# Optimization experiments

Measured on AMD Instinct MI355X. Metric: run time of the kernel, lower is better.

The kernel has to match this reference:

```python
import jax, jax.numpy as jnp
import numpy as np

H = 16            # num heads (sharded)
NOPE = 128        # qk_nope_head_dim
ROPE = 64         # qk_rope_head_dim
VD = 128          # v_head_dim
KV_RANK = 512
HEAD = NOPE + ROPE  # 192
SCALE = HEAD ** (-0.5)  # mscale == 1 (no yarn scaling)
EPS = 1e-6


def rmsnorm(x, w):
    var = jnp.mean(x * x, axis=-1, keepdims=True)
    return x * jax.lax.rsqrt(var + EPS) * w


def apply_rope(pe, cos, sin):
    # pe: [T, h, ROPE]; torch code de-interleaves pairs then applies
    # non-interleaved (rotate-half) rope: out = [e*cos - o*sin, o*cos + e*sin]
    e = pe[..., 0::2]
    o = pe[..., 1::2]
    c = cos[:, None, :]
    s = sin[:, None, :]
    return jnp.concatenate([e * c - o * s, o * c + e * s], axis=-1)


def setup_inputs() -> dict:
    key = jax.random.key(0)
    ks = jax.random.split(key, 10)
    T, D = 4096, 2048
    w = 0.02
    return {
        "hidden_states": jax.random.normal(ks[0], (T, D), jnp.float32),
        "cos": jax.random.uniform(ks[1], (T, ROPE // 2), jnp.float32),
        "sin": jax.random.uniform(ks[2], (T, ROPE // 2), jnp.float32),
        "w_q_a": jax.random.normal(ks[3], (D, 1536), jnp.float32) * w,
        "q_a_ln_w": jnp.ones((1536,), jnp.float32),
        "w_q_b": jax.random.normal(ks[4], (1536, H * HEAD), jnp.float32) * w,
        "w_kv_a": jax.random.normal(ks[5], (D, KV_RANK + ROPE), jnp.float32) * w,
        "kv_a_ln_w": jnp.ones((KV_RANK,), jnp.float32),
        "w_kv_b": jax.random.normal(ks[6], (KV_RANK, H * (NOPE + VD)), jnp.float32) * w,
        "w_o": jax.random.normal(ks[7], (H * VD, D), jnp.float32) * w,
        "batch_size": 2,
    }


def reference(hidden_states, cos, sin, w_q_a, q_a_ln_w, w_q_b, w_kv_a,
              kv_a_ln_w, w_kv_b, w_o, batch_size):
    T, D = hidden_states.shape
    B = int(batch_size)
    S = T // B

    # Q: low-rank down proj -> RMSNorm -> up proj
    q = rmsnorm(hidden_states @ w_q_a, q_a_ln_w) @ w_q_b
    q = q.reshape(T, H, HEAD)
    q_nope = q[..., :NOPE]
    q_pe = apply_rope(q[..., NOPE:], cos, sin)

    # KV: joint down proj with shared rope part (MQA-style)
    ckv = hidden_states @ w_kv_a                        # [T, 512+64]
    compressed_kv = ckv[:, :KV_RANK]
    k_pe = apply_rope(ckv[:, KV_RANK:][:, None, :], cos, sin)  # [T, 1, 64]
    kv = (rmsnorm(compressed_kv, kv_a_ln_w) @ w_kv_b).reshape(T, H, NOPE + VD)
    k_nope = kv[..., :NOPE]
    v = kv[..., NOPE:]                                   # [T, H, 128]

    # Assemble full query/key heads (value pad to 192 + final slice is a no-op
    # mathematically since padded dims are zero; we keep value dim = 128).
    query = jnp.concatenate([q_nope, q_pe], axis=-1)     # [T, H, 192]
    key = jnp.concatenate([k_nope, jnp.broadcast_to(k_pe, (T, H, ROPE))], axis=-1)

    # Causal (prefill) attention per sequence
    qb = query.reshape(B, S, H, HEAD)
    kb = key.reshape(B, S, H, HEAD)
    vb = v.reshape(B, S, H, VD)
    scores = jnp.einsum("bqhd,bkhd->bhqk", qb, kb) * SCALE
    causal = jnp.tril(jnp.ones((S, S), bool))
    scores = jnp.where(causal, scores, jnp.finfo(scores.dtype).min)
    probs = jax.nn.softmax(scores, axis=-1)
    attn = jnp.einsum("bhqk,bkhd->bqhd", probs, vb)      # [B, S, H, 128]

    return attn.reshape(T, H * VD) @ w_o
```

## Files before the change

### kernel.cpp

```cpp
#include <hip/hip_runtime.h>
#include <cstdint>
#include <cstddef>

#define TT 4096
#define DD 2048
#define NH 16
#define HEADD 192
#define NOPE 128
#define VDIM 128
#define SEQ 2048

typedef __bf16 bf16x8 __attribute__((ext_vector_type(8)));
typedef float f32x4 __attribute__((ext_vector_type(4)));
typedef unsigned int u32;

__device__ __forceinline__ float bf2f(unsigned short u) {
    union { unsigned int i; float f; } v; v.i = ((unsigned int)u) << 16; return v.f;
}
__device__ __forceinline__ unsigned short f2bf(float f) {
    union { float f; unsigned int i; } v; v.f = f;
    unsigned int r = v.i + 0x7FFFu + ((v.i >> 16) & 1u);
    return (unsigned short)(r >> 16);
}
__device__ __forceinline__ u32 pack2bf(float a, float b) {
    return (u32)f2bf(a) | ((u32)f2bf(b) << 16);
}
__device__ __forceinline__ void gload16(const unsigned short* g, unsigned short* l) {
    __builtin_amdgcn_global_load_lds((const __attribute__((address_space(1))) u32*)g,
                                     (__attribute__((address_space(3))) u32*)l, 16, 0, 0);
}

#define GMFMA __builtin_amdgcn_mfma_f32_16x16x32_bf16

__global__ __launch_bounds__(256) void cvt_bf16_k(const float* __restrict__ x,
                                                  unsigned short* __restrict__ y, int n) {
    int i = (blockIdx.x * 256 + threadIdx.x) * 4;
    if (i < n) {
        float4 v = *(const float4*)(x + i);
        uint2 o;
        o.x = pack2bf(v.x, v.y);
        o.y = pack2bf(v.z, v.w);
        *(uint2*)(y + i) = o;
    }
}

__global__ __launch_bounds__(256) void transpose_cvt_k(const float* __restrict__ W,
                                                       unsigned short* __restrict__ Wt,
                                                       int K, int N) {
    __shared__ float tile[32][33];
    int n0 = blockIdx.x * 32, k0 = blockIdx.y * 32;
    int t = threadIdx.x, lr = t >> 5, lc = t & 31;
#pragma unroll
    for (int p = 0; p < 4; p++) {
        int k = k0 + lr + p * 8, n = n0 + lc;
        tile[lr + p * 8][lc] = (k < K && n < N) ? W[(size_t)k * N + n] : 0.f;
    }
    __syncthreads();
#pragma unroll
    for (int p = 0; p < 4; p++) {
        int n = n0 + lr + p * 8, k = k0 + lc;
        if (n < N && k < K) Wt[(size_t)n * K + k] = f2bf(tile[lc][lr + p * 8]);
    }
}

template <int BN, typename OT>
__global__ __launch_bounds__(512) void gemm256_k(const unsigned short* __restrict__ A,
                                                 const unsigned short* __restrict__ Bt,
                                                 OT* __restrict__ C,
                                                 int M, int N, int K) {
    constexpr int NREP = BN / 64;
    constexpr int NB = BN / 64;
    constexpr int TILE_E = 8192 + BN * 64;
    __shared__ __align__(16) unsigned short lds[2 * TILE_E];
    const int t = threadIdx.x;
    const int w = t >> 6, lane = t & 63;
    const int wr = w >> 2, wc = w & 3;
    const int l15 = lane & 15, quad = lane >> 4;
    const int bm = blockIdx.y * 128, bn = blockIdx.x * BN;
    const int srow = w * 8 + (lane >> 3);
    const int scol = 8 * ((lane & 7) ^ (lane >> 3));
    const unsigned short* Ag = A + (size_t)(bm + srow) * K + scol;
    const unsigned short* Bg = Bt + (size_t)(bn + srow) * K + scol;
    const int rc0 = (quad * 8) ^ ((l15 & 7) * 8);
    const int rc1 = (32 + quad * 8) ^ ((l15 & 7) * 8);
    f32x4 acc[4][NREP];
    f32x4 zero = {0.f, 0.f, 0.f, 0.f};
#pragma unroll
    for (int i = 0; i < 4; i++)
#pragma unroll
        for (int n = 0; n < NREP; n++) acc[i][n] = zero;
    const int NT = K >> 6;
#pragma unroll
    for (int c = 0; c < 2; c++)
        gload16(Ag + (size_t)c * 64 * K, &lds[c * 4096 + w * 512]);
#pragma unroll
    for (int c = 0; c < NB; c++)
        gload16(Bg + (size_t)c * 64 * K, &lds[8192 + c * 4096 + w * 512]);

    for (int kt = 0; kt < NT; kt++) {
        const int cb = (kt & 1) * TILE_E;
        const int nb = TILE_E - cb;
        const bool more = (kt + 1) < NT;
        asm volatile("s_waitcnt vmcnt(0)" ::: "memory");
        __builtin_amdgcn_s_barrier();
        asm volatile("" ::: "memory");
        const unsigned short* Agk = Ag + (size_t)(kt + 1) * 64;
        const unsigned short* Bgk = Bg + (size_t)(kt + 1) * 64;
        if (more) {
            gload16(Agk, &lds[nb + w * 512]);
            gload16(Agk + (size_t)64 * K, &lds[nb + 4096 + w * 512]);
#pragma unroll
            for (int c = 0; c < NB / 2; c++)
                gload16(Bgk + (size_t)c * 64 * K, &lds[nb + 8192 + c * 4096 + w * 512]);
        }
        bf16x8 a0[2][2], b[NREP][2];
#pragma unroll
        for (int j = 0; j < 2; j++) {
            int rl = wr * 64 + j * 16 + l15;
            a0[j][0] = *(const bf16x8*)&lds[cb + rl * 64 + rc0];
            a0[j][1] = *(const bf16x8*)&lds[cb + rl * 64 + rc1];
        }
#pragma unroll
        for (int n = 0; n < NREP; n++) {
            int rl = wc * (BN / 4) + n * 16 + l15;
            b[n][0] = *(const bf16x8*)&lds[cb + 8192 + rl * 64 + rc0];
            b[n][1] = *(const bf16x8*)&lds[cb + 8192 + rl * 64 + rc1];
        }
        __builtin_amdgcn_s_setprio(1);
#pragma unroll
        for (int j = 0; j < 2; j++)
#pragma unroll
            for (int n = 0; n < NREP; n++) {
                acc[j][n] = GMFMA(a0[j][0], b[n][0], acc[j][n], 0, 0, 0);
                acc[j][n] = GMFMA(a0[j][1], b[n][1], acc[j][n], 0, 0, 0);
            }
        __builtin_amdgcn_s_setprio(0);
        __builtin_amdgcn_s_barrier();
        if (more) {
#pragma unroll
            for (int c = NB / 2; c < NB; c++)
                gload16(Bgk + (size_t)c * 64 * K, &lds[nb + 8192 + c * 4096 + w * 512]);
        }
        bf16x8 a1[2][2];
#pragma unroll
        for (int j = 0; j < 2; j++) {
            int rl = wr * 64 + 32 + j * 16 + l15;
            a1[j][0] = *(const bf16x8*)&lds[cb + rl * 64 + rc0];
            a1[j][1] = *(const bf16x8*)&lds[cb + rl * 64 + rc1];
        }
        __builtin_amdgcn_s_setprio(1);
#pragma unroll
        for (int j = 0; j < 2; j++)
#pragma unroll
            for (int n = 0; n < NREP; n++) {
                acc[2 + j][n] = GMFMA(a1[j][0], b[n][0], acc[2 + j][n], 0, 0, 0);
                acc[2 + j][n] = GMFMA(a1[j][1], b[n][1], acc[2 + j][n], 0, 0, 0);
            }
        __builtin_amdgcn_s_setprio(0);
    }
#pragma unroll
    for (int mi = 0; mi < 4; mi++) {
        int row = bm + wr * 64 + mi * 16 + quad * 4;
#pragma unroll
        for (int n = 0; n < NREP; n++) {
            int col = bn + wc * (BN / 4) + n * 16 + l15;
            OT* cp = C + (size_t)row * N + col;
#pragma unroll
            for (int r = 0; r < 4; r++) {
                float v = acc[mi][n][r];
                if constexpr (sizeof(OT) == 2) cp[(size_t)r * N] = f2bf(v);
                else                            cp[(size_t)r * N] = v;
            }
        }
    }
}

__global__ __launch_bounds__(512) void gemm192_rope_k(const unsigned short* __restrict__ A,
                                                      const unsigned short* __restrict__ Bt,
                                                      const float* __restrict__ cosb,
                                                      const float* __restrict__ sinb,
                                                      unsigned short* __restrict__ Qb) {
    constexpr int K = 1536, N = 3072;
    constexpr int NREP = 3, NB = 3;
    constexpr int TILE_E = 8192 + 192 * 64;
    __shared__ __align__(16) unsigned short lds[2 * TILE_E];
    const int t = threadIdx.x;
    const int w = t >> 6, lane = t & 63;
    const int wr = w >> 2, wc = w & 3;
    const int l15 = lane & 15, quad = lane >> 4;
    const int bm = blockIdx.y * 128, bn = blockIdx.x * 192;
    const int srow = w * 8 + (lane >> 3);
    const int scol = 8 * ((lane & 7) ^ (lane >> 3));
    const unsigned short* Ag = A + (size_t)(bm + srow) * K + scol;
    const unsigned short* Bg = Bt + (size_t)(bn + srow) * K + scol;
    const int rc0 = (quad * 8) ^ ((l15 & 7) * 8);
    const int rc1 = (32 + quad * 8) ^ ((l15 & 7) * 8);
    f32x4 acc[4][NREP];
    f32x4 zero = {0.f, 0.f, 0.f, 0.f};
#pragma unroll
    for (int i = 0; i < 4; i++)
#pragma unroll
        for (int n = 0; n < NREP; n++) acc[i][n] = zero;
    const int NT = K >> 6;
#pragma unroll
    for (int c = 0; c < 2; c++)
        gload16(Ag + (size_t)c * 64 * K, &lds[c * 4096 + w * 512]);
#pragma unroll
    for (int c = 0; c < NB; c++)
        gload16(Bg + (size_t)c * 64 * K, &lds[8192 + c * 4096 + w * 512]);

    for (int kt = 0; kt < NT; kt++) {
        const int cb = (kt & 1) * TILE_E;
        const int nb = TILE_E - cb;
        const bool more = (kt + 1) < NT;
        asm volatile("s_waitcnt vmcnt(0)" ::: "memory");
        __builtin_amdgcn_s_barrier();
        asm volatile("" ::: "memory");
        const unsigned short* Agk = Ag + (size_t)(kt + 1) * 64;
        const unsigned short* Bgk = Bg + (size_t)(kt + 1) * 64;
        if (more) {
            gload16(Agk, &lds[nb + w * 512]);
            gload16(Agk + (size_t)64 * K, &lds[nb + 4096 + w * 512]);
            gload16(Bgk, &lds[nb + 8192 + w * 512]);
        }
        bf16x8 a0[2][2], b[NREP][2];
#pragma unroll
        for (int j = 0; j < 2; j++) {
            int rl = wr * 64 + j * 16 + l15;
            a0[j][0] = *(const bf16x8*)&lds[cb + rl * 64 + rc0];
            a0[j][1] = *(const bf16x8*)&lds[cb + rl * 64 + rc1];
        }
#pragma unroll
        for (int n = 0; n < NREP; n++) {
            int rl = wc * 48 + n * 16 + l15;
            b[n][0] = *(const bf16x8*)&lds[cb + 8192 + rl * 64 + rc0];
            b[n][1] = *(const bf16x8*)&lds[cb + 8192 + rl * 64 + rc1];
        }
        __builtin_amdgcn_s_setprio(1);
#pragma unroll
        for (int j = 0; j < 2; j++)
#pragma unroll
            for (int n = 0; n < NREP; n++) {
                acc[j][n] = GMFMA(a0[j][0], b[n][0], acc[j][n], 0, 0, 0);
                acc[j][n] = GMFMA(a0[j][1], b[n][1], acc[j][n], 0, 0, 0);
            }
        __builtin_amdgcn_s_setprio(0);
        __builtin_amdgcn_s_barrier();
        if (more) {
#pragma unroll
            for (int c = 1; c < NB; c++)
                gload16(Bgk + (size_t)c * 64 * K, &lds[nb + 8192 + c * 4096 + w * 512]);
        }
        bf16x8 a1[2][2];
#pragma unroll
        for (int j = 0; j < 2; j++) {
            int rl = wr * 64 + 32 + j * 16 + l15;
            a1[j][0] = *(const bf16x8*)&lds[cb + rl * 64 + rc0];
            a1[j][1] = *(const bf16x8*)&lds[cb + rl * 64 + rc1];
        }
        __builtin_amdgcn_s_setprio(1);
#pragma unroll
        for (int j = 0; j < 2; j++)
#pragma unroll
            for (int n = 0; n < NREP; n++) {
                acc[2 + j][n] = GMFMA(a1[j][0], b[n][0], acc[2 + j][n], 0, 0, 0);
                acc[2 + j][n] = GMFMA(a1[j][1], b[n][1], acc[2 + j][n], 0, 0, 0);
            }
        __builtin_amdgcn_s_setprio(0);
    }
    __syncthreads();
    unsigned short* Ct = lds;
#pragma unroll
    for (int mi = 0; mi < 4; mi++) {
        int rl = wr * 64 + mi * 16 + quad * 4;
#pragma unroll
        for (int n = 0; n < NREP; n++) {
            int cl = wc * 48 + n * 16 + l15;
#pragma unroll
            for (int r = 0; r < 4; r++)
                Ct[(rl + r) * 200 + cl] = f2bf(acc[mi][n][r]);
        }
    }
    __syncthreads();
    {
        int r = t >> 2, cg = t & 3;
        int trow = bm + r;
        int h = blockIdx.x;
        const float* cr = cosb + (size_t)trow * 32;
        const float* sn = sinb + (size_t)trow * 32;
        unsigned short* dst = Qb + ((size_t)trow * NH + h) * HEADD + cg * 48;
        __align__(16) unsigned short tmp[48];
        const unsigned short* rowp = &Ct[r * 200];
        if (cg < 2) {
#pragma unroll
            for (int i = 0; i < 48; i++) tmp[i] = rowp[cg * 48 + i];
        } else if (cg == 2) {
#pragma unroll
            for (int i = 0; i < 32; i++) tmp[i] = rowp[96 + i];
            const unsigned short* pe = rowp + 128;
#pragma unroll
            for (int jj = 0; jj < 16; jj++) {
                float e = bf2f(pe[2 * jj]), o = bf2f(pe[2 * jj + 1]);
                tmp[32 + jj] = f2bf(e * cr[jj] - o * sn[jj]);
            }
        } else {
            const unsigned short* pe = rowp + 128;
#pragma unroll
            for (int jj = 16; jj < 32; jj++) {
                float e = bf2f(pe[2 * jj]), o = bf2f(pe[2 * jj + 1]);
                tmp[jj - 16] = f2bf(e * cr[jj] - o * sn[jj]);
            }
#pragma unroll
            for (int jj = 0; jj < 32; jj++) {
                float e = bf2f(pe[2 * jj]), o = bf2f(pe[2 * jj + 1]);
                tmp[16 + jj] = f2bf(o * cr[jj] + e * sn[jj]);
            }
        }
#pragma unroll
        for (int g = 0; g < 6; g++)
            *(uint4*)(dst + g * 8) = *(const uint4*)(&tmp[g * 8]);
    }
}

#define KS_STRIDE 192
#define VT_STRIDE 64
#define CS_STRIDE 132

__global__ __launch_bounds__(256) void gemm_kv_k(const unsigned short* __restrict__ A,
                                                 const unsigned short* __restrict__ Bt,
                                                 const unsigned short* __restrict__ kpe,
                                                 unsigned short* __restrict__ Kb2,
                                                 unsigned short* __restrict__ Vt2) {
    const int K = 512;
    __shared__ __align__(16) unsigned short smem[128 * CS_STRIDE];
    unsigned short* As = smem;
    unsigned short* Bs = smem + 128 * 32;
    unsigned short* Cs = smem;
    int bm = blockIdx.y * 128, bn = blockIdx.x * 128;
    int t = threadIdx.x;
    int wave = t >> 6, lane = t & 63;
    int wr = (wave >> 1) * 64, wc = (wave & 1) * 64;
    int l15 = lane & 15, quad = lane >> 4;
    f32x4 acc[4][4];
    f32x4 zero = {0.f, 0.f, 0.f, 0.f};
#pragma unroll
    for (int i = 0; i < 4; i++)
#pragma unroll
        for (int j = 0; j < 4; j++) acc[i][j] = zero;
    int r0 = 16 * (2 * wave) + (lane >> 2);
    int cOff = (lane & 3) * 8;
    const unsigned short* gA0 = A + (size_t)(bm + r0) * K + cOff;
    const unsigned short* gA1 = A + (size_t)(bm + r0 + 16) * K + cOff;
    const unsigned short* gB0 = Bt + (size_t)(bn + r0) * K + cOff;
    const unsigned short* gB1 = Bt + (size_t)(bn + r0 + 16) * K + cOff;
    unsigned short* lA0 = &As[(2 * wave) * 512];
    unsigned short* lA1 = &As[(2 * wave + 1) * 512];
    unsigned short* lB0 = &Bs[(2 * wave) * 512];
    unsigned short* lB1 = &Bs[(2 * wave + 1) * 512];
    for (int k0 = 0; k0 < K; k0 += 32) {
        gload16(gA0 + k0, lA0);
        gload16(gA1 + k0, lA1);
        gload16(gB0 + k0, lB0);
        gload16(gB1 + k0, lB1);
        __syncthreads();
        bf16x8 af[4], bfr[4];
#pragma unroll
        for (int i = 0; i < 4; i++)
            af[i] = *(const bf16x8*)&As[(wr + i * 16 + l15) * 32 + quad * 8];
#pragma unroll
        for (int j = 0; j < 4; j++)
            bfr[j] = *(const bf16x8*)&Bs[(wc + j * 16 + l15) * 32 + quad * 8];
#pragma unroll
        for (int i = 0; i < 4; i++)
#pragma unroll
            for (int j = 0; j < 4; j++)
                acc[i][j] = GMFMA(af[i], bfr[j], acc[i][j], 0, 0, 0);
        __syncthreads();
    }
#pragma unroll
    for (int i = 0; i < 4; i++) {
        int lr = wr + i * 16 + quad * 4;
#pragma unroll
        for (int j = 0; j < 4; j++) {
            int lc = wc + j * 16 + l15;
#pragma unroll
            for (int r = 0; r < 4; r++)
                Cs[(lr + r) * CS_STRIDE + lc] = f2bf(acc[i][j][r]);
        }
    }
    __syncthreads();
    int hh = bn >> 8;
    bool isV = (bn & 255) != 0;
    if (!isV) {
        int row = t >> 1, halfc = t & 1;
        int gs = bm + row;
        int b2 = gs >> 11, s2 = gs & 2047;
        int srl = s2 & 63, key = srl & 7;
        unsigned short* dpb = Kb2 +
            ((size_t)((b2 * NH + hh) * 32 + (s2 >> 6)) * 64 + srl) * KS_STRIDE;
        const unsigned short* sp = &Cs[row * CS_STRIDE + halfc * 64];
#pragma unroll
        for (int g = 0; g < 8; g++) {
            int dg = (halfc * 8 + g) ^ key;
            *(uint4*)(dpb + dg * 8) = *(const uint4*)(sp + g * 8);
        }
        if (halfc) {
            const unsigned short* kp = kpe + (size_t)gs * 64;
#pragma unroll
            for (int g = 0; g < 8; g++) {
                int dg = 16 + (g ^ key);
                *(uint4*)(dpb + dg * 8) = *(const uint4*)(kp + g * 8);
            }
        }
    } else {
        int kth = t >> 7, dim = t & 127;
        int gs0 = bm + kth * 64;
        int b2 = gs0 >> 11, s20 = gs0 & 2047;
        int keyv = dim & 7;
        unsigned short* dp = Vt2 +
            ((size_t)((b2 * NH + hh) * 32 + (s20 >> 6)) * 128 + dim) * VT_STRIDE;
#pragma unroll
        for (int g = 0; g < 8; g++) {
            uint4 o;
            unsigned short* op = (unsigned short*)&o;
#pragma unroll
            for (int q2 = 0; q2 < 8; q2++)
                op[q2] = Cs[(kth * 64 + g * 8 + q2) * CS_STRIDE + dim];
            *(uint4*)(dp + (g ^ keyv) * 8) = o;
        }
    }
}

__global__ __launch_bounds__(256) void norms_k(const unsigned short* __restrict__ qab,
                                               const float* __restrict__ qw,
                                               const float* __restrict__ kw,
                                               const float* __restrict__ cosb,
                                               const float* __restrict__ sinb,
                                               unsigned short* __restrict__ qan,
                                               unsigned short* __restrict__ ckvn,
                                               unsigned short* __restrict__ kpe) {
    const float QSCALE = 0.07216878364870323f;
    int row = blockIdx.x, t = threadIdx.x;
    const unsigned short* xr = qab + (size_t)row * 2304;
    float s1 = 0.f, s2 = 0.f;
    for (int i = t; i < 1536; i += 256) { float v = bf2f(xr[i]); s1 += v * v; }
#pragma unroll
    for (int i = t; i < 512; i += 256) { float v = bf2f(xr[1536 + i]); s2 += v * v; }
    __shared__ float r1[256], r2[256];
    r1[t] = s1; r2[t] = s2; __syncthreads();
    for (int o = 128; o > 0; o >>= 1) {
        if (t < o) { r1[t] += r1[t + o]; r2[t] += r2[t + o]; }
        __syncthreads();
    }
    float sc1 = rsqrtf(r1[0] / 1536.f + 1e-6f) * QSCALE;
    float sc2 = rsqrtf(r2[0] / 512.f + 1e-6f);
    unsigned short* y1 = qan + (size_t)row * 1536;
    for (int i = t; i < 1536; i += 256) y1[i] = f2bf(bf2f(xr[i]) * sc1 * qw[i]);
    unsigned short* y2 = ckvn + (size_t)row * 512;
#pragma unroll
    for (int i = t; i < 512; i += 256) y2[i] = f2bf(bf2f(xr[1536 + i]) * sc2 * kw[i]);
    if (t < 32) {
        float e = bf2f(xr[2048 + 2 * t]), o = bf2f(xr[2048 + 2 * t + 1]);
        float c = cosb[row * 32 + t], sn = sinb[row * 32 + t];
        kpe[row * 64 + t]      = f2bf(e * c - o * sn);
        kpe[row * 64 + 32 + t] = f2bf(o * c + e * sn);
    }
}

__global__ __launch_bounds__(512) void attn_mfma_k(const unsigned short* __restrict__ Qb,
                                                   const unsigned short* __restrict__ Kb2,
                                                   const unsigned short* __restrict__ Vt2,
                                                   unsigned short* __restrict__ Opart,
                                                   float* __restrict__ Mbuf,
                                                   float* __restrict__ Lbuf) {
    __shared__ __align__(16) unsigned short Ks[64 * KS_STRIDE];
    __shared__ __align__(16) unsigned short Vts[128 * VT_STRIDE];
    int xe = 39 - blockIdx.x;
    int h  = blockIdx.y;
    int b  = blockIdx.z;
    int qt = 0, accn = 0;
    while (true) { int c = (qt >> 2) + 1; if (xe < accn + c) break; accn += c; qt++; }
    int chunk = xe - accn;
    int t = threadIdx.x;
    int w = t >> 6, lane = t & 63;
    int l15 = lane & 15, quad = lane >> 4;
    int bh = b * NH + h;
    int q0 = b * SEQ + qt * 128;
    int qglob = qt * 128 + w * 16 + l15;
    int flat = bh * 40 + xe;
    const int kkey = l15 & 7;

    bf16x8 qf[6];
    {
        const unsigned short* qbase = Qb + ((size_t)(q0 + w * 16 + l15) * NH + h) * HEADD + quad * 8;
#pragma unroll
        for (int c = 0; c < 6; c++)
            qf[c] = *(const bf16x8*)(qbase + c * 32);
    }
    f32x4 acc_o[8];
    f32x4 zero = {0.f, 0.f, 0.f, 0.f};
#pragma unroll
    for (int j = 0; j < 8; j++) acc_o[j] = zero;
    float mrun = -1e30f, lrun = 0.f;

    int kt0 = chunk * 8, kt1 = min(kt0 + 7, 2 * qt + 1);
    int cbeg = w * 5;
    for (int kt = kt0; kt <= kt1; kt++) {
        __syncthreads();
        {
            const unsigned short* kg = Kb2 + ((size_t)bh * 32 + kt) * (64 * KS_STRIDE) + lane * 8;
            const unsigned short* vg = Vt2 + ((size_t)bh * 32 + kt) * (128 * VT_STRIDE) + lane * 8;
#pragma unroll
            for (int c = cbeg; c < cbeg + 5; c++) {
                if (c < 24) gload16(kg + c * 512, &Ks[c * 512]);
                else        gload16(vg + (c - 24) * 512, &Vts[(c - 24) * 512]);
            }
        }
        __syncthreads();
        f32x4 acc_s[4];
#pragma unroll
        for (int j = 0; j < 4; j++) acc_s[j] = zero;
#pragma unroll
        for (int c = 0; c < 6; c++) {
#pragma unroll
            for (int j = 0; j < 4; j++) {
                bf16x8 kf = *(const bf16x8*)&Ks[(j * 16 + l15) * KS_STRIDE + ((4 * c + quad) ^ kkey) * 8];
                acc_s[j] = GMFMA(kf, qf[c], acc_s[j], 0, 0, 0);
            }
        }
        float sv[4][4];
        const bool needmask = (kt * 64 + 63) > (qt * 128 + w * 16);
        if (needmask) {
#pragma unroll
            for (int j = 0; j < 4; j++) {
                int kbase = kt * 64 + j * 16 + quad * 4;
#pragma unroll
                for (int r = 0; r < 4; r++)
                    sv[j][r] = (kbase + r > qglob) ? -1e30f : acc_s[j][r];
            }
        } else {
#pragma unroll
            for (int j = 0; j < 4; j++)
#pragma unroll
                for (int r = 0; r < 4; r++) sv[j][r] = acc_s[j][r];
        }
        float v = sv[0][0];
#pragma unroll
        for (int j = 0; j < 4; j++)
#pragma unroll
            for (int r = 0; r < 4; r++) v = fmaxf(v, sv[j][r]);
        v = fmaxf(v, __shfl_xor(v, 16));
        v = fmaxf(v, __shfl_xor(v, 32));
        if (!__all(v - mrun <= 8.f)) {
            float mnew = fmaxf(mrun, v);
            float alpha = __expf(mrun - mnew);
            mrun = mnew;
            lrun *= alpha;
#pragma unroll
            for (int jt = 0; jt < 8; jt++)
#pragma unroll
                for (int r = 0; r < 4; r++) acc_o[jt][r] *= alpha;
        }
        float rs = 0.f;
#pragma unroll
        for (int j = 0; j < 4; j++)
#pragma unroll
            for (int r = 0; r < 4; r++) { float p = __expf(sv[j][r] - mrun); sv[j][r] = p; rs += p; }
        rs += __shfl_xor(rs, 16);
        rs += __shfl_xor(rs, 32);
        lrun += rs;
        u32 pk[4][2];
#pragma unroll
        for (int j = 0; j < 4; j++) {
            pk[j][0] = pack2bf(sv[j][0], sv[j][1]);
            pk[j][1] = pack2bf(sv[j][2], sv[j][3]);
        }
        int laneA = (((2 * quad) & 3) << 4) + l15;
        int laneB = (((2 * quad + 1) & 3) << 4) + l15;
        bool hi = (quad & 2) != 0;
#pragma unroll
        for (int c2 = 0; c2 < 2; c2++) {
            u32 a0 = __shfl(pk[2 * c2][0], laneA),     a1 = __shfl(pk[2 * c2][1], laneA);
            u32 b0 = __shfl(pk[2 * c2 + 1][0], laneA), b1 = __shfl(pk[2 * c2 + 1][1], laneA);
            u32 a2 = __shfl(pk[2 * c2][0], laneB),     a3 = __shfl(pk[2 * c2][1], laneB);
            u32 b2 = __shfl(pk[2 * c2 + 1][0], laneB), b3 = __shfl(pk[2 * c2 + 1][1], laneB);
            union { u32 d[4]; bf16x8 v8; } pf;
            pf.d[0] = hi ? b0 : a0;
            pf.d[1] = hi ? b1 : a1;
            pf.d[2] = hi ? b2 : a2;
            pf.d[3] = hi ? b3 : a3;
#pragma unroll
            for (int jt = 0; jt < 8; jt++) {
                bf16x8 vf = *(const bf16x8*)&Vts[(jt * 16 + l15) * VT_STRIDE + ((4 * c2 + quad) ^ kkey) * 8];
                acc_o[jt] = GMFMA(vf, pf.v8, acc_o[jt], 0, 0, 0);
            }
        }
    }
    {
        int row = w * 16 + l15;
        unsigned short* op = Opart + (size_t)flat * 16384 + row * 128;
#pragma unroll
        for (int jt = 0; jt < 8; jt++) {
            uint2 o;
            o.x = pack2bf(acc_o[jt][0], acc_o[jt][1]);
            o.y = pack2bf(acc_o[jt][2], acc_o[jt][3]);
            *(uint2*)(op + jt * 16 + quad * 4) = o;
        }
        if (quad == 0) {
            Mbuf[(size_t)flat * 128 + row] = mrun;
            Lbuf[(size_t)flat * 128 + row] = lrun;
        }
    }
}

__global__ __launch_bounds__(256) void attn_combine_k(const unsigned short* __restrict__ Opart,
                                                      const float* __restrict__ Mbuf,
                                                      const float* __restrict__ Lbuf,
                                                      unsigned short* __restrict__ attnb) {
    int q64 = blockIdx.x, h = blockIdx.y, b = blockIdx.z;
    int qt = q64 >> 1, half = q64 & 1;
    int nch = (qt >> 2) + 1;
    int F = 0;
    for (int q = 0; q < qt; q++) F += (q >> 2) + 1;
    int flat0 = (b * NH + h) * 40 + F;
    int t = threadIdx.x;
    int row = t >> 2, d0 = (t & 3) * 32;
    int row128 = half * 64 + row;
    float mc[4], lc[4], wgt[4];
    float mstar = -1e30f;
#pragma unroll
    for (int c = 0; c < 4; c++) {
        if (c < nch) {
            mc[c] = Mbuf[(size_t)(flat0 + c) * 128 + row128];
            lc[c] = Lbuf[(size_t)(flat0 + c) * 128 + row128];
        } else { mc[c] = -1e30f; lc[c] = 0.f; }
        mstar = fmaxf(mstar, mc[c]);
    }
    float L = 0.f;
#pragma unroll
    for (int c = 0; c < 4; c++) { wgt[c] = __expf(mc[c] - mstar); L += wgt[c] * lc[c]; }
    float invL = 1.f / L;
    float acc[32];
#pragma unroll
    for (int j = 0; j < 32; j++) acc[j] = 0.f;
#pragma unroll
    for (int c = 0; c < 4; c++) {
        if (c < nch) {
            const unsigned short* src = Opart + (size_t)(flat0 + c) * 16384 + row128 * 128 + d0;
            float wc = wgt[c];
#pragma unroll
            for (int g = 0; g < 4; g++) {
                uint4 u = *(const uint4*)(src + g * 8);
                const unsigned short* sp = (const unsigned short*)&u;
#pragma unroll
                for (int j = 0; j < 8; j++) acc[g * 8 + j] += wc * bf2f(sp[j]);
            }
        }
    }
    unsigned short* dst = attnb + (size_t)(b * SEQ + q64 * 64 + row) * 2048 + h * 128 + d0;
#pragma unroll
    for (int g = 0; g < 4; g++) {
        uint4 o;
        unsigned short* sp = (unsigned short*)&o;
#pragma unroll
        for (int j = 0; j < 8; j++) sp[j] = f2bf(acc[g * 8 + j] * invL);
        *(uint4*)(dst + g * 8) = o;
    }
}

extern "C" void kernel_launch(void* const* d_in, const int* in_sizes, int n_in,
                              void* d_out, int out_size, void* d_ws, size_t ws_size,
                              hipStream_t stream) {
    const float* hs     = (const float*)d_in[0];
    const float* cosb   = (const float*)d_in[1];
    const float* sinb   = (const float*)d_in[2];
    const float* w_q_a  = (const float*)d_in[3];
    const float* q_ln   = (const float*)d_in[4];
    const float* w_q_b  = (const float*)d_in[5];
    const float* w_kv_a = (const float*)d_in[6];
    const float* kv_ln  = (const float*)d_in[7];
    const float* w_kv_b = (const float*)d_in[8];
    const float* w_o    = (const float*)d_in[9];
    float* out = (float*)d_out;

    char* base = (char*)d_ws;
    size_t off = 0;
    auto take = [&](size_t bytes) { void* p = base + off; off += (bytes + 255) & ~(size_t)255; return p; };
    unsigned short* wqabT = (unsigned short*)take((size_t)2304 * 2048 * 2);
    unsigned short* wqbT  = (unsigned short*)take((size_t)3072 * 1536 * 2);
    unsigned short* wkvbT = (unsigned short*)take((size_t)4096 * 512 * 2);
    unsigned short* woT   = (unsigned short*)take((size_t)2048 * 2048 * 2);
    unsigned short* hsb   = (unsigned short*)take((size_t)TT * DD * 2);
    unsigned short* qab   = (unsigned short*)take((size_t)TT * 2304 * 2);
    unsigned short* qan   = (unsigned short*)take((size_t)TT * 1536 * 2);
    unsigned short* ckvn  = (unsigned short*)take((size_t)TT * 512 * 2);
    unsigned short* kpe   = (unsigned short*)take((size_t)TT * 64 * 2);
    unsigned short* Qbuf  = (unsigned short*)take((size_t)TT * NH * HEADD * 2);
    unsigned short* Kb2   = (unsigned short*)take((size_t)32 * 32 * 64 * KS_STRIDE * 2);
    unsigned short* Vt2   = (unsigned short*)take((size_t)32 * 32 * 128 * VT_STRIDE * 2);
    unsigned short* attnb = (unsigned short*)take((size_t)TT * 2048 * 2);
    unsigned short* Opart = (unsigned short*)take((size_t)1280 * 16384 * 2);
    float* Mbuf = (float*)take((size_t)1280 * 128 * 4);
    float* Lbuf = (float*)take((size_t)1280 * 128 * 4);

    cvt_bf16_k<<<(TT * DD) / 1024, 256, 0, stream>>>(hs, hsb, TT * DD);
    transpose_cvt_k<<<dim3(1536 / 32, 2048 / 32), 256, 0, stream>>>(w_q_a, wqabT, 2048, 1536);
    transpose_cvt_k<<<dim3(18, 2048 / 32), 256, 0, stream>>>(w_kv_a, wqabT + (size_t)1536 * 2048, 2048, 576);
    transpose_cvt_k<<<dim3(3072 / 32, 1536 / 32), 256, 0, stream>>>(w_q_b, wqbT, 1536, 3072);
    transpose_cvt_k<<<dim3(4096 / 32, 512 / 32), 256, 0, stream>>>(w_kv_b, wkvbT, 512, 4096);
    transpose_cvt_k<<<dim3(2048 / 32, 2048 / 32), 256, 0, stream>>>(w_o, woT, 2048, 2048);

    gemm256_k<256, unsigned short><<<dim3(9, 32), 512, 0, stream>>>(hsb, wqabT, qab, 4096, 2304, 2048);
    norms_k<<<4096, 256, 0, stream>>>(qab, q_ln, kv_ln, cosb, sinb, qan, ckvn, kpe);
    gemm192_rope_k<<<dim3(16, 32), 512, 0, stream>>>(qan, wqbT, cosb, sinb, Qbuf);
    gemm_kv_k<<<dim3(32, 32), 256, 0, stream>>>(ckvn, wkvbT, kpe, Kb2, Vt2);
    attn_mfma_k<<<dim3(40, 16, 2), 512, 0, stream>>>(Qbuf, Kb2, Vt2, Opart, Mbuf, Lbuf);
    attn_combine_k<<<dim3(32, 16, 2), 256, 0, stream>>>(Opart, Mbuf, Lbuf, attnb);
    gemm256_k<256, float><<<dim3(8, 32), 512, 0, stream>>>(attnb, woT, out, 4096, 2048, 2048);
}
```

Before: 519.5 us.

## Double-buffer K/V tiles in attention kernel with async prefetch of next tile

The attention kernel now allocates two LDS buffers for K and V tiles and issues the global-to-LDS loads for tile kt+1 before computing on tile kt. Explicit vmcnt waits and raw s_barrier calls replace the old load-then-sync pattern, so memory latency can overlap with the MFMA work. This doubles LDS use, which may lower occupancy. Correctness now depends on the hand-written waitcnt counts matching the number of outstanding loads.

```diff
diff --git a/kernel.cpp b/kernel.cpp
--- a/kernel.cpp
+++ b/kernel.cpp
@@ -473,8 +473,8 @@
                                                    unsigned short* __restrict__ Opart,
                                                    float* __restrict__ Mbuf,
                                                    float* __restrict__ Lbuf) {
-    __shared__ __align__(16) unsigned short Ks[64 * KS_STRIDE];
-    __shared__ __align__(16) unsigned short Vts[128 * VT_STRIDE];
+    __shared__ __align__(16) unsigned short Ks[2][64 * KS_STRIDE];
+    __shared__ __align__(16) unsigned short Vts[2][128 * VT_STRIDE];
     int xe = 39 - blockIdx.x;
     int h  = blockIdx.y;
     int b  = blockIdx.z;
@@ -490,6 +490,21 @@
     int flat = bh * 40 + xe;
     const int kkey = l15 & 7;
 
+    int kt0 = chunk * 8, kt1 = min(kt0 + 7, 2 * qt + 1);
+    const int nit = kt1 - kt0;
+    const int cbeg = w * 5;
+    const unsigned short* kgb = Kb2 + (size_t)(bh * 32) * (64 * KS_STRIDE) + lane * 8;
+    const unsigned short* vgb = Vt2 + (size_t)(bh * 32) * (128 * VT_STRIDE) + lane * 8;
+
+    {
+        const unsigned short* kg = kgb + (size_t)kt0 * (64 * KS_STRIDE);
+        const unsigned short* vg = vgb + (size_t)kt0 * (128 * VT_STRIDE);
+#pragma unroll
+        for (int c = cbeg; c < cbeg + 5; c++) {
+            if (c < 24) gload16(kg + c * 512, &Ks[0][c * 512]);
+            else        gload16(vg + (c - 24) * 512, &Vts[0][(c - 24) * 512]);
+        }
+    }
     bf16x8 qf[6];
     {
         const unsigned short* qbase = Qb + ((size_t)(q0 + w * 16 + l15) * NH + h) * HEADD + quad * 8;
@@ -503,20 +518,24 @@
     for (int j = 0; j < 8; j++) acc_o[j] = zero;
     float mrun = -1e30f, lrun = 0.f;
 
-    int kt0 = chunk * 8, kt1 = min(kt0 + 7, 2 * qt + 1);
-    int cbeg = w * 5;
-    for (int kt = kt0; kt <= kt1; kt++) {
-        __syncthreads();
-        {
-            const unsigned short* kg = Kb2 + ((size_t)bh * 32 + kt) * (64 * KS_STRIDE) + lane * 8;
-            const unsigned short* vg = Vt2 + ((size_t)bh * 32 + kt) * (128 * VT_STRIDE) + lane * 8;
+    for (int it = 0; it <= nit; it++) {
+        const int kt = kt0 + it;
+        const int p = it & 1;
+        const bool more = it < nit;
+        if (more) {
+            const unsigned short* kg = kgb + (size_t)(kt + 1) * (64 * KS_STRIDE);
+            const unsigned short* vg = vgb + (size_t)(kt + 1) * (128 * VT_STRIDE);
 #pragma unroll
             for (int c = cbeg; c < cbeg + 5; c++) {
-                if (c < 24) gload16(kg + c * 512, &Ks[c * 512]);
-                else        gload16(vg + (c - 24) * 512, &Vts[(c - 24) * 512]);
-            }
-        }
-        __syncthreads();
+                if (c < 24) gload16(kg + c * 512, &Ks[p ^ 1][c * 512]);
+                else        gload16(vg + (c - 24) * 512, &Vts[p ^ 1][(c - 24) * 512]);
+            }
+            asm volatile("s_waitcnt vmcnt(5)" ::: "memory");
+        } else {
+            asm volatile("s_waitcnt vmcnt(0)" ::: "memory");
+        }
+        __builtin_amdgcn_s_barrier();
+        asm volatile("" ::: "memory");
         f32x4 acc_s[4];
 #pragma unroll
         for (int j = 0; j < 4; j++) acc_s[j] = zero;
@@ -524,7 +543,7 @@
         for (int c = 0; c < 6; c++) {
 #pragma unroll
             for (int j = 0; j < 4; j++) {
-                bf16x8 kf = *(const bf16x8*)&Ks[(j * 16 + l15) * KS_STRIDE + ((4 * c + quad) ^ kkey) * 8];
+                bf16x8 kf = *(const bf16x8*)&Ks[p][(j * 16 + l15) * KS_STRIDE + ((4 * c + quad) ^ kkey) * 8];
                 acc_s[j] = GMFMA(kf, qf[c], acc_s[j], 0, 0, 0);
             }
         }
@@ -565,7 +584,7 @@
 #pragma unroll
         for (int j = 0; j < 4; j++)
 #pragma unroll
-            for (int r = 0; r < 4; r++) { float p = __expf(sv[j][r] - mrun); sv[j][r] = p; rs += p; }
+            for (int r = 0; r < 4; r++) { float pp = __expf(sv[j][r] - mrun); sv[j][r] = pp; rs += pp; }
         rs += __shfl_xor(rs, 16);
         rs += __shfl_xor(rs, 32);
         lrun += rs;
@@ -591,10 +610,12 @@
             pf.d[3] = hi ? b3 : a3;
 #pragma unroll
             for (int jt = 0; jt < 8; jt++) {
-                bf16x8 vf = *(const bf16x8*)&Vts[(jt * 16 + l15) * VT_STRIDE + ((4 * c2 + quad) ^ kkey) * 8];
+                bf16x8 vf = *(const bf16x8*)&Vts[p][(jt * 16 + l15) * VT_STRIDE + ((4 * c2 + quad) ^ kkey) * 8];
                 acc_o[jt] = GMFMA(vf, pf.v8, acc_o[jt], 0, 0, 0);
             }
         }
+        asm volatile("" ::: "memory");
+        __builtin_amdgcn_s_barrier();
     }
     {
         int row = w * 16 + l15;
```

New measurement: 509.6 us. About the same (-1.9%).
